# Kernel optimization log

Hardware: AMD Instinct MI355X
Metric: run time of the kernel (lower is better)

Reference implementation:

```python
import jax, jax.numpy as jnp
import numpy as np

N, E, D, L, POS_VOC = 50000, 800000, 128, 3, 1024
EPS = 1e-5  # torch LayerNorm default


def layer_norm(x, g, b):
    m = jnp.mean(x, axis=-1, keepdims=True)
    v = jnp.var(x, axis=-1, keepdims=True)
    return (x - m) * jax.lax.rsqrt(v + EPS) * g + b


def setup_inputs() -> dict:
    key = jax.random.key(0)
    ks = jax.random.split(key, 8)
    node_emb = jax.random.normal(ks[0], (N, D), jnp.float32)
    pos = jax.random.randint(ks[1], (N,), 0, POS_VOC, dtype=jnp.int32)
    edge = jax.random.randint(ks[2], (2, E), 0, N, dtype=jnp.int32)
    # pos_embedding: xavier-uniform rows 1:, padding_idx=0 row zeroed
    lim = np.sqrt(6.0 / (POS_VOC - 1 + D))
    pos_table = jax.random.uniform(ks[3], (POS_VOC, D), jnp.float32, -lim, lim)
    pos_table = pos_table.at[0].set(0.0)
    # SAGEConv per layer: lin_l (with bias) on aggregated neighbors, lin_r (no bias) on root
    Wl = jax.random.normal(ks[4], (L, D, D), jnp.float32) / np.sqrt(D)
    bl = jnp.zeros((L, D), jnp.float32)
    Wr = jax.random.normal(ks[5], (L, D, D), jnp.float32) / np.sqrt(D)
    emb_ln_g = jnp.ones((D,), jnp.float32)
    emb_ln_b = jnp.zeros((D,), jnp.float32)
    hid_ln_g = jnp.ones((L, D), jnp.float32)
    hid_ln_b = jnp.zeros((L, D), jnp.float32)
    return dict(node_emb=node_emb, pos=pos, edge=edge, pos_table=pos_table,
                Wl=Wl, bl=bl, Wr=Wr, emb_ln_g=emb_ln_g, emb_ln_b=emb_ln_b,
                hid_ln_g=hid_ln_g, hid_ln_b=hid_ln_b)


def reference(node_emb, pos, edge, pos_table, Wl, bl, Wr,
              emb_ln_g, emb_ln_b, hid_ln_g, hid_ln_b):
    # embedding: scaled node emb + position embedding, then LayerNorm (dropout p=0 -> identity)
    x = node_emb * np.float32(np.sqrt(D)) + pos_table[pos]        # [N, D]
    x = layer_norm(x, emb_ln_g, emb_ln_b)
    src, dst = edge[0], edge[1]
    for i in range(L):
        # SAGEConv(aggr='add'): scatter-add neighbor feats, transform, add root transform
        agg = jax.ops.segment_sum(x[src], dst, num_segments=N)    # [N, D]
        h = agg @ Wl[i] + bl[i] + x @ Wr[i]                       # [N, D]
        h = jax.nn.relu(h)
        x = layer_norm(h + x, hid_ln_g[i], hid_ln_b[i])           # residual + LN
    return x
```

## Files before the change

### kernel.cpp

```cpp
#include <hip/hip_runtime.h>

#define DDIM    128
#define NNODES  50000
#define NEDGES  800000
#define NLAYERS 3
#define LN_EPS  1e-5f
#define CAP     96
#define NSLICE  8
#define SLICESZ ((NNODES + NSLICE - 1) / NSLICE)
#define FILL_EPT 8
#define FILL_CHUNK (256 * FILL_EPT)
#define FILL_NCHUNK ((NEDGES + FILL_CHUNK - 1) / FILL_CHUNK)

#define FILLB  (FILL_NCHUNK * NSLICE)
#define WPACKB ((NLAYERS * 4096 + 255) / 256)
#define EMBEDB ((NNODES + 15) / 16)

typedef short s16x8 __attribute__((ext_vector_type(8)));
typedef float f32x4 __attribute__((ext_vector_type(4)));
typedef unsigned int u32;

__device__ __forceinline__ unsigned short f2bf(float f) {
    union { float f; unsigned u; } c; c.f = f;
    unsigned r = c.u + 0x7fff + ((c.u >> 16) & 1);
    return (unsigned short)(r >> 16);
}
__device__ __forceinline__ float bf2f_u(unsigned short h) {
    union { unsigned u; float f; } c; c.u = (unsigned)h << 16;
    return c.f;
}
__device__ __forceinline__ float bflo(u32 v) { return __uint_as_float(v << 16); }
__device__ __forceinline__ float bfhi(u32 v) { return __uint_as_float(v & 0xffff0000u); }

__global__ __launch_bounds__(256) void prep_kernel(
    const int* __restrict__ edge,
    int* __restrict__ cursor, int* __restrict__ srcs,
    const float* __restrict__ Wl, const float* __restrict__ Wr,
    unsigned short* __restrict__ wpk,
    const float* __restrict__ node_emb, const int* __restrict__ pos,
    const float* __restrict__ pos_table,
    const float* __restrict__ eg, const float* __restrict__ eb,
    uint4* __restrict__ xh4)
{
    int t = threadIdx.x;

    if (blockIdx.x < FILLB) {
        int slice = blockIdx.x & (NSLICE - 1);
        int chunk = blockIdx.x >> 3;
        int lo = slice * SLICESZ;
        int hi = lo + SLICESZ;
        int base = chunk * FILL_CHUNK + t * FILL_EPT;
        if (base < NEDGES) {
            int4 d0 = *(const int4*)(edge + NEDGES + base);
            int4 d1 = *(const int4*)(edge + NEDGES + base + 4);
            int4 s0 = *(const int4*)(edge + base);
            int4 s1 = *(const int4*)(edge + base + 4);
            int dd[8] = {d0.x, d0.y, d0.z, d0.w, d1.x, d1.y, d1.z, d1.w};
            int ss[8] = {s0.x, s0.y, s0.z, s0.w, s1.x, s1.y, s1.z, s1.w};
            #pragma unroll
            for (int i = 0; i < 8; ++i) {
                int d = dd[i];
                if (d >= lo && d < hi) {
                    int slot = atomicAdd(&cursor[d], 1);
                    srcs[d * CAP + slot] = ss[i];
                }
            }
        }
        return;
    }

    if (blockIdx.x < FILLB + WPACKB) {
        int idx = (blockIdx.x - FILLB) * 256 + t;
        if (idx >= NLAYERS * 4096) return;
        int l   = idx >> 12;
        int rem = idx & 4095;
        int kt = rem >> 9, ct = (rem >> 6) & 7, ln = rem & 63;
        int k0 = kt * 32 + ((ln >> 4) << 3);
        int c  = ct * 16 + (ln & 15);
        const float* src = (kt < 4)
            ? Wl + (size_t)l * DDIM * DDIM + (size_t)k0 * DDIM + c
            : Wr + (size_t)l * DDIM * DDIM + (size_t)(k0 - 128) * DDIM + c;
        s16x8 o;
        #pragma unroll
        for (int j = 0; j < 8; ++j) o[j] = (short)f2bf(src[j * DDIM]);
        *(s16x8*)(wpk + (size_t)idx * 8) = o;
        return;
    }

    int bi = blockIdx.x - FILLB - WPACKB;
    int wv = (bi * 256 + t) >> 6;
    int lane = t & 63;
    int h = lane >> 4;
    int L = lane & 15;
    int n = wv * 4 + h;
    if (n >= NNODES) return;

    const float scale = 11.313708498984761f;
    int p = pos[n];

    const float* nb = node_emb + (size_t)n * DDIM + L * 8;
    const float* pb = pos_table + (size_t)p * DDIM + L * 8;
    float4 ne0 = *(const float4*)(nb);
    float4 ne1 = *(const float4*)(nb + 4);
    float4 pt0 = *(const float4*)(pb);
    float4 pt1 = *(const float4*)(pb + 4);

    float v[8];
    v[0] = ne0.x * scale + pt0.x;  v[1] = ne0.y * scale + pt0.y;
    v[2] = ne0.z * scale + pt0.z;  v[3] = ne0.w * scale + pt0.w;
    v[4] = ne1.x * scale + pt1.x;  v[5] = ne1.y * scale + pt1.y;
    v[6] = ne1.z * scale + pt1.z;  v[7] = ne1.w * scale + pt1.w;

    float s = 0.f, s2 = 0.f;
    #pragma unroll
    for (int k = 0; k < 8; ++k) { s += v[k]; s2 += v[k] * v[k]; }
    #pragma unroll
    for (int m = 8; m > 0; m >>= 1) {
        s  += __shfl_xor(s,  m, 64);
        s2 += __shfl_xor(s2, m, 64);
    }
    float mean = s * (1.0f / DDIM);
    float var  = s2 * (1.0f / DDIM) - mean * mean;
    float rstd = rsqrtf(var + LN_EPS);

    float4 gv0 = *(const float4*)(eg + L * 8);
    float4 gv1 = *(const float4*)(eg + L * 8 + 4);
    float4 bv0 = *(const float4*)(eb + L * 8);
    float4 bv1 = *(const float4*)(eb + L * 8 + 4);
    float gq[8] = {gv0.x, gv0.y, gv0.z, gv0.w, gv1.x, gv1.y, gv1.z, gv1.w};
    float bq[8] = {bv0.x, bv0.y, bv0.z, bv0.w, bv1.x, bv1.y, bv1.z, bv1.w};

    float y[8];
    #pragma unroll
    for (int k = 0; k < 8; ++k) y[k] = (v[k] - mean) * rstd * gq[k] + bq[k];

    uint4 o;
    o.x = (u32)f2bf(y[0]) | ((u32)f2bf(y[1]) << 16);
    o.y = (u32)f2bf(y[2]) | ((u32)f2bf(y[3]) << 16);
    o.z = (u32)f2bf(y[4]) | ((u32)f2bf(y[5]) << 16);
    o.w = (u32)f2bf(y[6]) | ((u32)f2bf(y[7]) << 16);
    xh4[(size_t)n * 16 + L] = o;
}

__global__ __launch_bounds__(256) void sage_fused_kernel(
    const int* __restrict__ deg,
    const int* __restrict__ srcs,
    const uint4* __restrict__ xin4,
    const unsigned short* __restrict__ xin,
    const unsigned short* __restrict__ wpk,
    const float* __restrict__ bl,
    const float* __restrict__ g,
    const float* __restrict__ b,
    unsigned short* __restrict__ xh_out,
    float* __restrict__ xout)
{
    __shared__ unsigned short wlds[4096 * 8];
    __shared__ uint4 aggl[64 * 16];

    int t    = threadIdx.x;
    int wave = t >> 6;
    int lane = t & 63;
    int cl   = lane & 15;
    int q    = lane >> 4;

    {
        const s16x8* srcv = (const s16x8*)wpk;
        s16x8* dstv = (s16x8*)wlds;
        #pragma unroll
        for (int i = 0; i < 16; ++i) dstv[t + i * 256] = srcv[t + i * 256];
    }

    int m0 = blockIdx.x * 64;

    for (int r = 0; r < 4; ++r) {
        int nl = wave * 16 + r * 4 + q;
        int n  = m0 + nl;
        float acc[8];
        #pragma unroll
        for (int k = 0; k < 8; ++k) acc[k] = 0.f;
        if (n < NNODES) {
            int dg  = deg[n];
            int beg = n * CAP;
            for (int j = 0; j < dg; j += 8) {
                int sidx[8];
                #pragma unroll
                for (int c = 0; c < 8; ++c) {
                    int jj = j + c;
                    sidx[c] = (jj < dg) ? srcs[beg + jj] : -1;
                }
                uint4 u[8];
                #pragma unroll
                for (int c = 0; c < 8; ++c) {
                    u[c] = make_uint4(0u, 0u, 0u, 0u);
                    if (sidx[c] >= 0) u[c] = xin4[(size_t)sidx[c] * 16 + cl];
                }
                #pragma unroll
                for (int c = 0; c < 8; ++c) {
                    acc[0] += bflo(u[c].x); acc[1] += bfhi(u[c].x);
                    acc[2] += bflo(u[c].y); acc[3] += bfhi(u[c].y);
                    acc[4] += bflo(u[c].z); acc[5] += bfhi(u[c].z);
                    acc[6] += bflo(u[c].w); acc[7] += bfhi(u[c].w);
                }
            }
        }
        uint4 o;
        o.x = (u32)f2bf(acc[0]) | ((u32)f2bf(acc[1]) << 16);
        o.y = (u32)f2bf(acc[2]) | ((u32)f2bf(acc[3]) << 16);
        o.z = (u32)f2bf(acc[4]) | ((u32)f2bf(acc[5]) << 16);
        o.w = (u32)f2bf(acc[6]) | ((u32)f2bf(acc[7]) << 16);
        aggl[nl * 16 + (cl ^ (nl & 7))] = o;
    }
    __syncthreads();

    float bias[8], gg[8], bb[8];
    #pragma unroll
    for (int ct = 0; ct < 8; ++ct) {
        int c = ct * 16 + cl;
        bias[ct] = bl[c]; gg[ct] = g[c]; bb[ct] = b[c];
    }

    int wbase = m0 + wave * 16;
    int mrow  = wave * 16 + cl;
    int m  = wbase + cl;
    int mc = (m < NNODES) ? m : (NNODES - 1);

    s16x8 af[8];
    #pragma unroll
    for (int kt = 0; kt < 4; ++kt)
        af[kt] = *(const s16x8*)&aggl[mrow * 16 + ((kt * 4 + q) ^ (cl & 7))];
    #pragma unroll
    for (int kt = 4; kt < 8; ++kt)
        af[kt] = *(const s16x8*)(xin + (size_t)mc * DDIM + (kt - 4) * 32 + q * 8);

    f32x4 accm[8];
    #pragma unroll
    for (int ct = 0; ct < 8; ++ct) accm[ct] = (f32x4){0.f, 0.f, 0.f, 0.f};

    #pragma unroll
    for (int kt = 0; kt < 8; ++kt) {
        #pragma unroll
        for (int ct = 0; ct < 8; ++ct) {
            s16x8 bfr = *(const s16x8*)&wlds[((((kt << 3) + ct) << 6) + lane) * 8];
            accm[ct] = __builtin_amdgcn_mfma_f32_16x16x32_bf16(af[kt], bfr, accm[ct], 0, 0, 0);
        }
    }

    float hbuf[8][4];
    #pragma unroll
    for (int ct = 0; ct < 8; ++ct) {
        #pragma unroll
        for (int rr = 0; rr < 4; ++rr) {
            int node = wbase + q * 4 + rr;
            int nc   = (node < NNODES) ? node : (NNODES - 1);
            float hv = fmaxf(accm[ct][rr] + bias[ct], 0.0f);
            hbuf[ct][rr] = hv + bf2f_u(xin[(size_t)nc * DDIM + ct * 16 + cl]);
        }
    }

    float s[4], s2[4];
    #pragma unroll
    for (int rr = 0; rr < 4; ++rr) {
        float a0 = 0.f, a1 = 0.f;
        #pragma unroll
        for (int ct = 0; ct < 8; ++ct) {
            a0 += hbuf[ct][rr];
            a1 += hbuf[ct][rr] * hbuf[ct][rr];
        }
        #pragma unroll
        for (int msk = 1; msk < 16; msk <<= 1) {
            a0 += __shfl_xor(a0, msk, 64);
            a1 += __shfl_xor(a1, msk, 64);
        }
        s[rr] = a0; s2[rr] = a1;
    }

    #pragma unroll
    for (int rr = 0; rr < 4; ++rr) {
        int node = wbase + q * 4 + rr;
        if (node >= NNODES) continue;
        float mean = s[rr] * (1.0f / DDIM);
        float var  = s2[rr] * (1.0f / DDIM) - mean * mean;
        float rstd = rsqrtf(var + LN_EPS);
        #pragma unroll
        for (int ct = 0; ct < 8; ++ct) {
            float y = (hbuf[ct][rr] - mean) * rstd * gg[ct] + bb[ct];
            size_t off = (size_t)node * DDIM + ct * 16 + cl;
            if (xout) xout[off]    = y;
            else      xh_out[off]  = f2bf(y);
        }
    }
}

extern "C" void kernel_launch(void* const* d_in, const int* in_sizes, int n_in,
                              void* d_out, int out_size, void* d_ws, size_t ws_size,
                              hipStream_t stream)
{
    const float* node_emb = (const float*)d_in[0];
    const int*   pos      = (const int*)d_in[1];
    const int*   edge     = (const int*)d_in[2];
    const float* pos_tab  = (const float*)d_in[3];
    const float* Wl       = (const float*)d_in[4];
    const float* bl       = (const float*)d_in[5];
    const float* Wr       = (const float*)d_in[6];
    const float* eg       = (const float*)d_in[7];
    const float* eb       = (const float*)d_in[8];
    const float* hg       = (const float*)d_in[9];
    const float* hb       = (const float*)d_in[10];

    unsigned short* xA  = (unsigned short*)d_ws;
    unsigned short* xB  = xA + (size_t)NNODES * DDIM;
    unsigned short* wpk = xB + (size_t)NNODES * DDIM;
    int* cursor = (int*)(wpk + (size_t)NLAYERS * 4096 * 8);
    int* srcs   = cursor + NNODES;

    hipMemsetAsync(cursor, 0, NNODES * sizeof(int), stream);
    prep_kernel<<<FILLB + WPACKB + EMBEDB, 256, 0, stream>>>(
        edge, cursor, srcs, Wl, Wr, wpk,
        node_emb, pos, pos_tab, eg, eb, (uint4*)xA);

    for (int l = 0; l < NLAYERS; ++l) {
        unsigned short* xin = (l & 1) ? xB : xA;
        unsigned short* xo  = (l & 1) ? xA : xB;
        sage_fused_kernel<<<(NNODES + 63) / 64, 256, 0, stream>>>(
            cursor, srcs, (const uint4*)xin, xin,
            wpk + (size_t)l * 4096 * 8,
            bl + (size_t)l * DDIM,
            hg + (size_t)l * DDIM,
            hb + (size_t)l * DDIM,
            xo, (l == NLAYERS - 1) ? (float*)d_out : (float*)nullptr);
    }
}
```

Before: 280.7 us.

## Stream weights through smaller LDS buffer in quarters to raise occupancy

Result: faster. 248.4 us (-11.5%).

```diff
diff --git a/kernel.cpp b/kernel.cpp
--- a/kernel.cpp
+++ b/kernel.cpp
@@ -142,7 +142,7 @@
     xh4[(size_t)n * 16 + L] = o;
 }
 
-__global__ __launch_bounds__(256) void sage_fused_kernel(
+__global__ __launch_bounds__(256, 4) void sage_fused_kernel(
     const int* __restrict__ deg,
     const int* __restrict__ srcs,
     const uint4* __restrict__ xin4,
@@ -154,7 +154,7 @@
     unsigned short* __restrict__ xh_out,
     float* __restrict__ xout)
 {
-    __shared__ unsigned short wlds[4096 * 8];
+    __shared__ unsigned short wlds[8192];
     __shared__ uint4 aggl[64 * 16];
 
     int t    = threadIdx.x;
@@ -167,7 +167,7 @@
         const s16x8* srcv = (const s16x8*)wpk;
         s16x8* dstv = (s16x8*)wlds;
         #pragma unroll
-        for (int i = 0; i < 16; ++i) dstv[t + i * 256] = srcv[t + i * 256];
+        for (int i = 0; i < 4; ++i) dstv[t + i * 256] = srcv[t + i * 256];
     }
 
     int m0 = blockIdx.x * 64;
@@ -210,39 +210,54 @@
         o.w = (u32)f2bf(acc[6]) | ((u32)f2bf(acc[7]) << 16);
         aggl[nl * 16 + (cl ^ (nl & 7))] = o;
     }
-    __syncthreads();
-
-    float bias[8], gg[8], bb[8];
-    #pragma unroll
-    for (int ct = 0; ct < 8; ++ct) {
-        int c = ct * 16 + cl;
-        bias[ct] = bl[c]; gg[ct] = g[c]; bb[ct] = b[c];
-    }
 
     int wbase = m0 + wave * 16;
     int mrow  = wave * 16 + cl;
     int m  = wbase + cl;
     int mc = (m < NNODES) ? m : (NNODES - 1);
 
-    s16x8 af[8];
-    #pragma unroll
-    for (int kt = 0; kt < 4; ++kt)
-        af[kt] = *(const s16x8*)&aggl[mrow * 16 + ((kt * 4 + q) ^ (cl & 7))];
+    s16x8 af47[4];
     #pragma unroll
     for (int kt = 4; kt < 8; ++kt)
-        af[kt] = *(const s16x8*)(xin + (size_t)mc * DDIM + (kt - 4) * 32 + q * 8);
+        af47[kt - 4] = *(const s16x8*)(xin + (size_t)mc * DDIM + (kt - 4) * 32 + q * 8);
+
+    __syncthreads();
 
     f32x4 accm[8];
     #pragma unroll
     for (int ct = 0; ct < 8; ++ct) accm[ct] = (f32x4){0.f, 0.f, 0.f, 0.f};
 
     #pragma unroll
-    for (int kt = 0; kt < 8; ++kt) {
-        #pragma unroll
-        for (int ct = 0; ct < 8; ++ct) {
-            s16x8 bfr = *(const s16x8*)&wlds[((((kt << 3) + ct) << 6) + lane) * 8];
-            accm[ct] = __builtin_amdgcn_mfma_f32_16x16x32_bf16(af[kt], bfr, accm[ct], 0, 0, 0);
-        }
+    for (int p = 0; p < 4; ++p) {
+        #pragma unroll
+        for (int kk = 0; kk < 2; ++kk) {
+            int kt = p * 2 + kk;
+            s16x8 af;
+            if (kt < 4)
+                af = *(const s16x8*)&aggl[mrow * 16 + ((kt * 4 + q) ^ (cl & 7))];
+            else
+                af = af47[kt - 4];
+            #pragma unroll
+            for (int ct = 0; ct < 8; ++ct) {
+                s16x8 bfr = *(const s16x8*)&wlds[((((kk << 3) + ct) << 6) + lane) * 8];
+                accm[ct] = __builtin_amdgcn_mfma_f32_16x16x32_bf16(af, bfr, accm[ct], 0, 0, 0);
+            }
+        }
+        __syncthreads();
+        if (p < 3) {
+            const s16x8* srcv = (const s16x8*)(wpk + (size_t)(p + 1) * 8192);
+            s16x8* dstv = (s16x8*)wlds;
+            #pragma unroll
+            for (int i = 0; i < 4; ++i) dstv[t + i * 256] = srcv[t + i * 256];
+            __syncthreads();
+        }
+    }
+
+    float bias[8], gg[8], bb[8];
+    #pragma unroll
+    for (int ct = 0; ct < 8; ++ct) {
+        int c = ct * 16 + cl;
+        bias[ct] = bl[c]; gg[ct] = g[c]; bb[ct] = b[c];
     }
 
     float hbuf[8][4];
```
